# Optimization experiments

Hardware: AMD Instinct MI355X
Metric: run time of the kernel (lower is better)

The kernel has to match this reference:

```python
import jax, jax.numpy as jnp
import numpy as np

EMBED_DIM = 1024
HEAD_SIZE = 128
B, S = 8, 2048

def setup_inputs() -> dict:
    rng = jax.random.key(0)
    k1, k2, k3, k4, k5, k6 = jax.random.split(rng, 6)
    std = 1.0 / EMBED_DIM  # nn.initializers.normal(stddev=1/embed_dim)
    return {
        "key": jax.random.normal(k1, (B, S, EMBED_DIM), dtype=jnp.float32),
        "query": jax.random.normal(k2, (B, S, EMBED_DIM), dtype=jnp.float32),
        "value": jax.random.normal(k3, (B, S, EMBED_DIM), dtype=jnp.float32),
        "W_Q": jax.random.normal(k4, (EMBED_DIM, HEAD_SIZE), dtype=jnp.float32) * std,
        "W_K": jax.random.normal(k5, (EMBED_DIM, HEAD_SIZE), dtype=jnp.float32) * std,
        "W_V": jax.random.normal(k6, (EMBED_DIM, HEAD_SIZE), dtype=jnp.float32) * std,
    }

def reference(key, query, value, W_Q, W_K, W_V):
    # Parallel retention: (Q K^T * causal_mask) V
    q_proj = query @ W_Q        # (B, S, H)
    k_proj = key @ W_K          # (B, S, H)
    v_proj = value @ W_V        # (B, S, H)
    ret = jnp.einsum("bsh,bth->bst", q_proj, k_proj)  # (B, S, S)
    # full_self_retention=False -> lower-triangular (causal) mask
    decay_matrix = jnp.tril(jnp.ones((S, S), dtype=ret.dtype))
    ret = ret * decay_matrix
    return ret @ v_proj          # (B, S, H)
```

## Files before the change

### kernel.cpp

```cpp
#include <hip/hip_runtime.h>
#include <cstdint>

#define B_  8
#define S_  2048
#define E_  1024
#define H_  128
#define NC_ 16

typedef __attribute__((ext_vector_type(8))) short bf16x8;
typedef __attribute__((ext_vector_type(4))) float f32x4;

__device__ __forceinline__ short f2bf(float f){
  uint32_t u = __builtin_bit_cast(uint32_t, f);
  u = (u + 0x7fffu + ((u >> 16) & 1u)) >> 16;
  return (short)u;
}
__device__ __forceinline__ float bf2f(short s){
  uint32_t u = ((uint32_t)(uint16_t)s) << 16;
  return __builtin_bit_cast(float, u);
}

__global__ __launch_bounds__(256) void wt_kernel(
    const float* __restrict__ WQ, const float* __restrict__ WK,
    const float* __restrict__ WV,
    short* __restrict__ WtQ, short* __restrict__ WtK, short* __restrict__ WtV)
{
  int which = blockIdx.z;
  const float* W = which == 0 ? WQ : which == 1 ? WK : WV;
  short* Wt      = which == 0 ? WtQ : which == 1 ? WtK : WtV;
  int k0 = blockIdx.x * 32, n0 = blockIdx.y * 32;
  __shared__ float t[32][33];
  int tx = threadIdx.x & 31, ty = threadIdx.x >> 5;
  #pragma unroll
  for (int i = 0; i < 4; i++)
    t[ty + i * 8][tx] = W[(size_t)(k0 + ty + i * 8) * H_ + n0 + tx];
  __syncthreads();
  #pragma unroll
  for (int i = 0; i < 4; i++)
    Wt[(size_t)(n0 + ty + i * 8) * E_ + k0 + tx] = f2bf(t[tx][ty + i * 8]);
}

__global__ __launch_bounds__(256) void proj_kernel(
    const float* __restrict__ Xq, const float* __restrict__ Xk,
    const float* __restrict__ Xv,
    const short* __restrict__ Wtq, const short* __restrict__ Wtk,
    const short* __restrict__ Wtv,
    short* __restrict__ q, short* __restrict__ k,
    short* __restrict__ kT, short* __restrict__ vT)
{
  int which = blockIdx.y;
  const float* X  = which == 0 ? Xq  : which == 1 ? Xk  : Xv;
  const short* Wt = which == 0 ? Wtq : which == 1 ? Wtk : Wtv;

  int tid = threadIdx.x, lane = tid & 63, wave = tid >> 6;
  int lr = lane & 15, lq = lane >> 4;
  int rowbase = blockIdx.x * 64 + wave * 16;

  __shared__ short Bs[2][128 * 72];

  const float* xr = X + (size_t)(rowbase + lr) * E_ + lq * 8;

  f32x4 acc[8];
  #pragma unroll
  for (int tn = 0; tn < 8; tn++) acc[tn] = (f32x4){0.f, 0.f, 0.f, 0.f};

  bf16x8 bst[4];
  f32x4  a0[4], a1[4];

  #pragma unroll
  for (int v = 0; v < 4; v++){
    int c = v * 256 + tid;
    int n = c >> 3, off = (c & 7) * 8;
    bst[v] = *(const bf16x8*)(Wt + (size_t)n * E_ + off);
  }
  #pragma unroll
  for (int s = 0; s < 2; s++){
    a0[2 * s]     = *(const f32x4*)(xr + s * 32);
    a0[2 * s + 1] = *(const f32x4*)(xr + s * 32 + 4);
  }
  #pragma unroll
  for (int v = 0; v < 4; v++){
    int c = v * 256 + tid;
    int n = c >> 3, off = (c & 7) * 8;
    *(bf16x8*)(&Bs[0][n * 72 + off]) = bst[v];
  }
  __syncthreads();

  for (int t = 0; t < 16; t++){
    const int cur = t & 1;
    if (t < 15){
      #pragma unroll
      for (int v = 0; v < 4; v++){
        int c = v * 256 + tid;
        int n = c >> 3, off = (c & 7) * 8;
        bst[v] = *(const bf16x8*)(Wt + (size_t)n * E_ + (t + 1) * 64 + off);
      }
      #pragma unroll
      for (int s = 0; s < 2; s++){
        a1[2 * s]     = *(const f32x4*)(xr + (t + 1) * 64 + s * 32);
        a1[2 * s + 1] = *(const f32x4*)(xr + (t + 1) * 64 + s * 32 + 4);
      }
    }
    #pragma unroll
    for (int s = 0; s < 2; s++){
      bf16x8 a;
      #pragma unroll
      for (int j = 0; j < 4; j++){
        a[j] = f2bf(a0[2 * s][j]); a[4 + j] = f2bf(a0[2 * s + 1][j]);
      }
      #pragma unroll
      for (int tn = 0; tn < 8; tn++){
        bf16x8 bfr = *(const bf16x8*)(&Bs[cur][(tn * 16 + lr) * 72 + s * 32 + lq * 8]);
        acc[tn] = __builtin_amdgcn_mfma_f32_16x16x32_bf16(a, bfr, acc[tn], 0, 0, 0);
      }
    }
    if (t < 15){
      #pragma unroll
      for (int v = 0; v < 4; v++){
        int c = v * 256 + tid;
        int n = c >> 3, off = (c & 7) * 8;
        *(bf16x8*)(&Bs[cur ^ 1][n * 72 + off]) = bst[v];
      }
      #pragma unroll
      for (int i2 = 0; i2 < 4; i2++) a0[i2] = a1[i2];
      __syncthreads();
    }
  }

  if (which <= 1){
    short* P = which == 0 ? q : k;
    #pragma unroll
    for (int tn = 0; tn < 8; tn++)
      #pragma unroll
      for (int r4 = 0; r4 < 4; r4++)
        P[(size_t)(rowbase + lq * 4 + r4) * H_ + tn * 16 + lr] = f2bf(acc[tn][r4]);
  }
  if (which >= 1){
    short* T = which == 1 ? kT : vT;
    int b = rowbase >> 11, srow = rowbase & 2047;
    #pragma unroll
    for (int tn = 0; tn < 8; tn++){
      union { short sh[4]; uint2 u; } pk;
      #pragma unroll
      for (int r4 = 0; r4 < 4; r4++) pk.sh[r4] = f2bf(acc[tn][r4]);
      *(uint2*)(T + ((size_t)b * H_ + tn * 16 + lr) * S_ + srow + lq * 4) = pk.u;
    }
  }
}

__global__ __launch_bounds__(256) void chunk_state(
    const short* __restrict__ vT, const short* __restrict__ kT,
    float* __restrict__ M)
{
  int j = blockIdx.x, half = blockIdx.y, b = blockIdx.z;
  int tid = threadIdx.x, lane = tid & 63, wave = tid >> 6;
  int wrow = wave * 32;
  int lr = lane & 15, lq = lane >> 4;

  __shared__ short As[128 * 136];
  __shared__ short Bs[64 * 136];

  const short* vtb = vT + (size_t)b * H_ * S_ + j * 128;
  const short* ktb = kT + (size_t)b * H_ * S_ + (size_t)half * 64 * S_ + j * 128;

  #pragma unroll
  for (int v = 0; v < 8; v++){
    int c = v * 256 + tid;
    int r = c >> 4, off = (c & 15) * 8;
    *(bf16x8*)(&As[r * 136 + off]) = *(const bf16x8*)(vtb + (size_t)r * S_ + off);
  }
  #pragma unroll
  for (int v = 0; v < 4; v++){
    int c = v * 256 + tid;
    int r = c >> 4, off = (c & 15) * 8;
    *(bf16x8*)(&Bs[r * 136 + off]) = *(const bf16x8*)(ktb + (size_t)r * S_ + off);
  }
  __syncthreads();

  f32x4 acc[2][4];
  #pragma unroll
  for (int a = 0; a < 2; a++)
    #pragma unroll
    for (int c = 0; c < 4; c++) acc[a][c] = (f32x4){0.f, 0.f, 0.f, 0.f};

  #pragma unroll
  for (int s = 0; s < 4; s++){
    int t0 = s * 32;
    bf16x8 af[2], bf[4];
    #pragma unroll
    for (int tm = 0; tm < 2; tm++)
      af[tm] = *(const bf16x8*)(&As[(wrow + tm * 16 + lr) * 136 + t0 + lq * 8]);
    #pragma unroll
    for (int tn = 0; tn < 4; tn++)
      bf[tn] = *(const bf16x8*)(&Bs[(tn * 16 + lr) * 136 + t0 + lq * 8]);
    #pragma unroll
    for (int tm = 0; tm < 2; tm++)
      #pragma unroll
      for (int tn = 0; tn < 4; tn++)
        acc[tm][tn] = __builtin_amdgcn_mfma_f32_16x16x32_bf16(
            af[tm], bf[tn], acc[tm][tn], 0, 0, 0);
  }

  float* mb = M + (size_t)(b * NC_ + j) * 16384;
  #pragma unroll
  for (int tm = 0; tm < 2; tm++)
    #pragma unroll
    for (int tn = 0; tn < 4; tn++)
      #pragma unroll
      for (int r4 = 0; r4 < 4; r4++){
        int row = wrow + tm * 16 + lq * 4 + r4;
        int col = half * 64 + tn * 16 + lr;
        mb[row * 128 + col] = acc[tm][tn][r4];
      }
}

__global__ __launch_bounds__(256) void prefix_state(
    const float* __restrict__ M, short* __restrict__ Shi, short* __restrict__ Slo)
{
  int b = blockIdx.y;
  int idx = (blockIdx.x * 256 + threadIdx.x) * 2;
  float2 mv[NC_];
  #pragma unroll
  for (int j = 0; j < NC_; j++)
    mv[j] = *(const float2*)(M + (size_t)(b * NC_ + j) * 16384 + idx);

  float r0 = 0.f, r1 = 0.f;
  #pragma unroll
  for (int j = 0; j < NC_; j++){
    size_t o = (size_t)(b * NC_ + j) * 16384 + idx;
    short h0 = f2bf(r0), h1 = f2bf(r1);
    short l0 = f2bf(r0 - bf2f(h0)), l1 = f2bf(r1 - bf2f(h1));
    union { short s[2]; uint32_t u; } ph, pl;
    ph.s[0] = h0; ph.s[1] = h1;
    pl.s[0] = l0; pl.s[1] = l1;
    *(uint32_t*)(Shi + o) = ph.u;
    *(uint32_t*)(Slo + o) = pl.u;
    r0 += mv[j].x; r1 += mv[j].y;
  }
}

__global__ __launch_bounds__(256) void passC(
    const short* __restrict__ qb, const short* __restrict__ kb,
    const short* __restrict__ vT, const short* __restrict__ Shi,
    const short* __restrict__ Slo, float* __restrict__ out)
{
  int i = blockIdx.x, half = blockIdx.y, b = blockIdx.z;
  int roff = half * 64;
  int tid = threadIdx.x, lane = tid & 63, wave = tid >> 6;
  int wrow = (wave >> 1) * 32, wcol = (wave & 1) * 64;
  int lr = lane & 15, lq = lane >> 4;

  __shared__ short Ss[64 * 136];
  __shared__ short Bt0[128 * 136];
  __shared__ short Bt1[128 * 136];

  const short* qbase = qb + ((size_t)b * S_ + i * 128 + roff) * H_;
  const short* kbase = kb + ((size_t)b * S_ + i * 128) * H_;
  const short* vtb   = vT + (size_t)b * H_ * S_ + i * 128;
  const short* shib  = Shi + (size_t)(b * NC_ + i) * 16384;
  const short* slob  = Slo + (size_t)(b * NC_ + i) * 16384;

  bf16x8 kst[8], vst[8], hst[8], lst[8];
  #pragma unroll
  for (int v = 0; v < 8; v++){
    int c = v * 256 + tid;
    int r = c >> 4, off = (c & 15) * 8;
    kst[v] = *(const bf16x8*)(kbase + (size_t)r * H_ + off);
    vst[v] = *(const bf16x8*)(vtb  + (size_t)r * S_ + off);
    hst[v] = *(const bf16x8*)(shib + (size_t)r * 128 + off);
    lst[v] = *(const bf16x8*)(slob + (size_t)r * 128 + off);
  }
  bf16x8 aq[2][4];
  #pragma unroll
  for (int tm = 0; tm < 2; tm++)
    #pragma unroll
    for (int hs = 0; hs < 4; hs++)
      aq[tm][hs] = *(const bf16x8*)(
          qbase + (size_t)(wrow + tm * 16 + lr) * H_ + hs * 32 + lq * 8);

  #pragma unroll
  for (int v = 0; v < 8; v++){
    int c = v * 256 + tid;
    int r = c >> 4, off = (c & 15) * 8;
    *(bf16x8*)(&Bt0[r * 136 + off]) = kst[v];
  }
  __syncthreads();

  f32x4 acc[2][4];
  #pragma unroll
  for (int a = 0; a < 2; a++)
    #pragma unroll
    for (int c = 0; c < 4; c++) acc[a][c] = (f32x4){0.f, 0.f, 0.f, 0.f};

  #pragma unroll
  for (int hs = 0; hs < 4; hs++){
    bf16x8 bf[4];
    #pragma unroll
    for (int tn = 0; tn < 4; tn++)
      bf[tn] = *(const bf16x8*)(&Bt0[(wcol + tn * 16 + lr) * 136 + hs * 32 + lq * 8]);
    #pragma unroll
    for (int tm = 0; tm < 2; tm++)
      #pragma unroll
      for (int tn = 0; tn < 4; tn++)
        acc[tm][tn] = __builtin_amdgcn_mfma_f32_16x16x32_bf16(
            aq[tm][hs], bf[tn], acc[tm][tn], 0, 0, 0);
  }

  #pragma unroll
  for (int tm = 0; tm < 2; tm++)
    #pragma unroll
    for (int tn = 0; tn < 4; tn++)
      #pragma unroll
      for (int r4 = 0; r4 < 4; r4++){
        int row = wrow + tm * 16 + lq * 4 + r4;
        int col = wcol + tn * 16 + lr;
        float vv = (col <= roff + row) ? acc[tm][tn][r4] : 0.f;
        Ss[row * 136 + col] = f2bf(vv);
      }
  #pragma unroll
  for (int v = 0; v < 8; v++){
    int c = v * 256 + tid;
    int r = c >> 4, off = (c & 15) * 8;
    *(bf16x8*)(&Bt1[r * 136 + off]) = vst[v];
  }
  #pragma unroll
  for (int a = 0; a < 2; a++)
    #pragma unroll
    for (int c = 0; c < 4; c++) acc[a][c] = (f32x4){0.f, 0.f, 0.f, 0.f};
  __syncthreads();

  #pragma unroll
  for (int s = 0; s < 4; s++){
    int t0 = s * 32;
    bf16x8 af[2], bf[4];
    #pragma unroll
    for (int tm = 0; tm < 2; tm++)
      af[tm] = *(const bf16x8*)(&Ss[(wrow + tm * 16 + lr) * 136 + t0 + lq * 8]);
    #pragma unroll
    for (int tn = 0; tn < 4; tn++)
      bf[tn] = *(const bf16x8*)(&Bt1[(wcol + tn * 16 + lr) * 136 + t0 + lq * 8]);
    #pragma unroll
    for (int tm = 0; tm < 2; tm++)
      #pragma unroll
      for (int tn = 0; tn < 4; tn++)
        acc[tm][tn] = __builtin_amdgcn_mfma_f32_16x16x32_bf16(
            af[tm], bf[tn], acc[tm][tn], 0, 0, 0);
  }
  #pragma unroll
  for (int v = 0; v < 8; v++){
    int c = v * 256 + tid;
    int r = c >> 4, off = (c & 15) * 8;
    *(bf16x8*)(&Bt0[r * 136 + off]) = hst[v];
  }
  __syncthreads();

  #pragma unroll
  for (int hs = 0; hs < 4; hs++){
    bf16x8 bf[4];
    #pragma unroll
    for (int tn = 0; tn < 4; tn++)
      bf[tn] = *(const bf16x8*)(&Bt0[(wcol + tn * 16 + lr) * 136 + hs * 32 + lq * 8]);
    #pragma unroll
    for (int tm = 0; tm < 2; tm++)
      #pragma unroll
      for (int tn = 0; tn < 4; tn++)
        acc[tm][tn] = __builtin_amdgcn_mfma_f32_16x16x32_bf16(
            aq[tm][hs], bf[tn], acc[tm][tn], 0, 0, 0);
  }
  #pragma unroll
  for (int v = 0; v < 8; v++){
    int c = v * 256 + tid;
    int r = c >> 4, off = (c & 15) * 8;
    *(bf16x8*)(&Bt1[r * 136 + off]) = lst[v];
  }
  __syncthreads();

  #pragma unroll
  for (int hs = 0; hs < 4; hs++){
    bf16x8 bf[4];
    #pragma unroll
    for (int tn = 0; tn < 4; tn++)
      bf[tn] = *(const bf16x8*)(&Bt1[(wcol + tn * 16 + lr) * 136 + hs * 32 + lq * 8]);
    #pragma unroll
    for (int tm = 0; tm < 2; tm++)
      #pragma unroll
      for (int tn = 0; tn < 4; tn++)
        acc[tm][tn] = __builtin_amdgcn_mfma_f32_16x16x32_bf16(
            aq[tm][hs], bf[tn], acc[tm][tn], 0, 0, 0);
  }

  float* ob = out + ((size_t)b * S_ + i * 128 + roff) * H_;
  #pragma unroll
  for (int tm = 0; tm < 2; tm++)
    #pragma unroll
    for (int tn = 0; tn < 4; tn++)
      #pragma unroll
      for (int r4 = 0; r4 < 4; r4++){
        int row = wrow + tm * 16 + lq * 4 + r4;
        int col = wcol + tn * 16 + lr;
        ob[(size_t)row * H_ + col] = acc[tm][tn][r4];
      }
}

extern "C" void kernel_launch(void* const* d_in, const int* in_sizes, int n_in,
                              void* d_out, int out_size, void* d_ws, size_t ws_size,
                              hipStream_t stream) {
  const float* key   = (const float*)d_in[0];
  const float* query = (const float*)d_in[1];
  const float* value = (const float*)d_in[2];
  const float* WQ    = (const float*)d_in[3];
  const float* WK    = (const float*)d_in[4];
  const float* WV    = (const float*)d_in[5];
  float* out = (float*)d_out;

  char* w = (char*)d_ws;
  short* WtQ = (short*)(w + 0);
  short* WtK = (short*)(w + 262144);
  short* WtV = (short*)(w + 524288);
  size_t o = 786432;
  short* q  = (short*)(w + o); o += 4194304;
  short* k  = (short*)(w + o); o += 4194304;
  short* kT = (short*)(w + o); o += 4194304;
  short* vT = (short*)(w + o); o += 4194304;
  float* M  = (float*)(w + o); o += 8388608;
  short* Shi= (short*)(w + o); o += 4194304;
  short* Slo= (short*)(w + o); o += 4194304;

  wt_kernel   <<<dim3(32, 4, 3),       256, 0, stream>>>(WQ, WK, WV, WtQ, WtK, WtV);
  proj_kernel <<<dim3(256, 3),         256, 0, stream>>>(query, key, value,
                                                         WtQ, WtK, WtV, q, k, kT, vT);
  chunk_state <<<dim3(NC_, 2, B_),     256, 0, stream>>>(vT, kT, M);
  prefix_state<<<dim3(32, B_),         256, 0, stream>>>(M, Shi, Slo);
  passC       <<<dim3(NC_, 2, B_),     256, 0, stream>>>(q, k, vT, Shi, Slo, out);
}
```

Before: 239.2 us.

## Drop LDS staging in projection and split chunk kernels into quarter tiles

The projection kernel now reads bf16 weight fragments straight from global memory (L2-resident) instead of double-buffering them through shared memory, which removes the barriers and LDS traffic. It also loads 128-wide K chunks per iteration. chunk_state and passC now split each 128-row chunk into four 32-row pieces instead of two 64-row pieces, doubling the grid (256 to 512 blocks) so the 256 CUs are better occupied. In exchange, passC re-stages the full K, V and state tiles four times per chunk, and the projection kernel makes more scattered global reads.

```diff
diff --git a/kernel.cpp b/kernel.cpp
--- a/kernel.cpp
+++ b/kernel.cpp
@@ -56,74 +56,34 @@
   int lr = lane & 15, lq = lane >> 4;
   int rowbase = blockIdx.x * 64 + wave * 16;
 
-  __shared__ short Bs[2][128 * 72];
-
   const float* xr = X + (size_t)(rowbase + lr) * E_ + lq * 8;
+  const short* wb = Wt + (size_t)lr * E_ + lq * 8;
 
   f32x4 acc[8];
   #pragma unroll
   for (int tn = 0; tn < 8; tn++) acc[tn] = (f32x4){0.f, 0.f, 0.f, 0.f};
 
-  bf16x8 bst[4];
-  f32x4  a0[4], a1[4];
-
-  #pragma unroll
-  for (int v = 0; v < 4; v++){
-    int c = v * 256 + tid;
-    int n = c >> 3, off = (c & 7) * 8;
-    bst[v] = *(const bf16x8*)(Wt + (size_t)n * E_ + off);
-  }
-  #pragma unroll
-  for (int s = 0; s < 2; s++){
-    a0[2 * s]     = *(const f32x4*)(xr + s * 32);
-    a0[2 * s + 1] = *(const f32x4*)(xr + s * 32 + 4);
-  }
-  #pragma unroll
-  for (int v = 0; v < 4; v++){
-    int c = v * 256 + tid;
-    int n = c >> 3, off = (c & 7) * 8;
-    *(bf16x8*)(&Bs[0][n * 72 + off]) = bst[v];
-  }
-  __syncthreads();
-
-  for (int t = 0; t < 16; t++){
-    const int cur = t & 1;
-    if (t < 15){
-      #pragma unroll
-      for (int v = 0; v < 4; v++){
-        int c = v * 256 + tid;
-        int n = c >> 3, off = (c & 7) * 8;
-        bst[v] = *(const bf16x8*)(Wt + (size_t)n * E_ + (t + 1) * 64 + off);
-      }
-      #pragma unroll
-      for (int s = 0; s < 2; s++){
-        a1[2 * s]     = *(const f32x4*)(xr + (t + 1) * 64 + s * 32);
-        a1[2 * s + 1] = *(const f32x4*)(xr + (t + 1) * 64 + s * 32 + 4);
-      }
+  #pragma unroll 2
+  for (int kc = 0; kc < 8; kc++){
+    f32x4 ar[8];
+    #pragma unroll
+    for (int s = 0; s < 4; s++){
+      ar[2 * s]     = *(const f32x4*)(xr + kc * 128 + s * 32);
+      ar[2 * s + 1] = *(const f32x4*)(xr + kc * 128 + s * 32 + 4);
     }
     #pragma unroll
-    for (int s = 0; s < 2; s++){
+    for (int s = 0; s < 4; s++){
       bf16x8 a;
       #pragma unroll
       for (int j = 0; j < 4; j++){
-        a[j] = f2bf(a0[2 * s][j]); a[4 + j] = f2bf(a0[2 * s + 1][j]);
+        a[j] = f2bf(ar[2 * s][j]); a[4 + j] = f2bf(ar[2 * s + 1][j]);
       }
       #pragma unroll
       for (int tn = 0; tn < 8; tn++){
-        bf16x8 bfr = *(const bf16x8*)(&Bs[cur][(tn * 16 + lr) * 72 + s * 32 + lq * 8]);
+        bf16x8 bfr = *(const bf16x8*)(
+            wb + (size_t)(tn * 16) * E_ + kc * 128 + s * 32);
         acc[tn] = __builtin_amdgcn_mfma_f32_16x16x32_bf16(a, bfr, acc[tn], 0, 0, 0);
       }
-    }
-    if (t < 15){
-      #pragma unroll
-      for (int v = 0; v < 4; v++){
-        int c = v * 256 + tid;
-        int n = c >> 3, off = (c & 7) * 8;
-        *(bf16x8*)(&Bs[cur ^ 1][n * 72 + off]) = bst[v];
-      }
-      #pragma unroll
-      for (int i2 = 0; i2 < 4; i2++) a0[i2] = a1[i2];
-      __syncthreads();
     }
   }
 
@@ -152,16 +112,16 @@
     const short* __restrict__ vT, const short* __restrict__ kT,
     float* __restrict__ M)
 {
-  int j = blockIdx.x, half = blockIdx.y, b = blockIdx.z;
+  int j = blockIdx.x, qtr = blockIdx.y, b = blockIdx.z;
   int tid = threadIdx.x, lane = tid & 63, wave = tid >> 6;
   int wrow = wave * 32;
   int lr = lane & 15, lq = lane >> 4;
 
   __shared__ short As[128 * 136];
-  __shared__ short Bs[64 * 136];
+  __shared__ short Bs[32 * 136];
 
   const short* vtb = vT + (size_t)b * H_ * S_ + j * 128;
-  const short* ktb = kT + (size_t)b * H_ * S_ + (size_t)half * 64 * S_ + j * 128;
+  const short* ktb = kT + (size_t)b * H_ * S_ + (size_t)qtr * 32 * S_ + j * 128;
 
   #pragma unroll
   for (int v = 0; v < 8; v++){
@@ -170,33 +130,33 @@
     *(bf16x8*)(&As[r * 136 + off]) = *(const bf16x8*)(vtb + (size_t)r * S_ + off);
   }
   #pragma unroll
-  for (int v = 0; v < 4; v++){
+  for (int v = 0; v < 2; v++){
     int c = v * 256 + tid;
     int r = c >> 4, off = (c & 15) * 8;
     *(bf16x8*)(&Bs[r * 136 + off]) = *(const bf16x8*)(ktb + (size_t)r * S_ + off);
   }
   __syncthreads();
 
-  f32x4 acc[2][4];
+  f32x4 acc[2][2];
   #pragma unroll
   for (int a = 0; a < 2; a++)
     #pragma unroll
-    for (int c = 0; c < 4; c++) acc[a][c] = (f32x4){0.f, 0.f, 0.f, 0.f};
+    for (int c = 0; c < 2; c++) acc[a][c] = (f32x4){0.f, 0.f, 0.f, 0.f};
 
   #pragma unroll
   for (int s = 0; s < 4; s++){
     int t0 = s * 32;
-    bf16x8 af[2], bf[4];
+    bf16x8 af[2], bf[2];
     #pragma unroll
     for (int tm = 0; tm < 2; tm++)
       af[tm] = *(const bf16x8*)(&As[(wrow + tm * 16 + lr) * 136 + t0 + lq * 8]);
     #pragma unroll
-    for (int tn = 0; tn < 4; tn++)
+    for (int tn = 0; tn < 2; tn++)
       bf[tn] = *(const bf16x8*)(&Bs[(tn * 16 + lr) * 136 + t0 + lq * 8]);
     #pragma unroll
     for (int tm = 0; tm < 2; tm++)
       #pragma unroll
-      for (int tn = 0; tn < 4; tn++)
+      for (int tn = 0; tn < 2; tn++)
         acc[tm][tn] = __builtin_amdgcn_mfma_f32_16x16x32_bf16(
             af[tm], bf[tn], acc[tm][tn], 0, 0, 0);
   }
@@ -205,11 +165,11 @@
   #pragma unroll
   for (int tm = 0; tm < 2; tm++)
     #pragma unroll
-    for (int tn = 0; tn < 4; tn++)
+    for (int tn = 0; tn < 2; tn++)
       #pragma unroll
       for (int r4 = 0; r4 < 4; r4++){
         int row = wrow + tm * 16 + lq * 4 + r4;
-        int col = half * 64 + tn * 16 + lr;
+        int col = qtr * 32 + tn * 16 + lr;
         mb[row * 128 + col] = acc[tm][tn][r4];
       }
 }
@@ -244,13 +204,13 @@
     const short* __restrict__ vT, const short* __restrict__ Shi,
     const short* __restrict__ Slo, float* __restrict__ out)
 {
-  int i = blockIdx.x, half = blockIdx.y, b = blockIdx.z;
-  int roff = half * 64;
+  int i = blockIdx.x, qtr = blockIdx.y, b = blockIdx.z;
+  int roff = qtr * 32;
   int tid = threadIdx.x, lane = tid & 63, wave = tid >> 6;
-  int wrow = (wave >> 1) * 32, wcol = (wave & 1) * 64;
+  int wcol = wave * 32;
   int lr = lane & 15, lq = lane >> 4;
 
-  __shared__ short Ss[64 * 136];
+  __shared__ short Ss[32 * 136];
   __shared__ short Bt0[128 * 136];
   __shared__ short Bt1[128 * 136];
 
@@ -276,7 +236,7 @@
     #pragma unroll
     for (int hs = 0; hs < 4; hs++)
       aq[tm][hs] = *(const bf16x8*)(
-          qbase + (size_t)(wrow + tm * 16 + lr) * H_ + hs * 32 + lq * 8);
+          qbase + (size_t)(tm * 16 + lr) * H_ + hs * 32 + lq * 8);
 
   #pragma unroll
   for (int v = 0; v < 8; v++){
@@ -286,117 +246,118 @@
   }
   __syncthreads();
 
-  f32x4 acc[2][4];
+  f32x4 accS[2][2];
   #pragma unroll
   for (int a = 0; a < 2; a++)
     #pragma unroll
-    for (int c = 0; c < 4; c++) acc[a][c] = (f32x4){0.f, 0.f, 0.f, 0.f};
+    for (int c = 0; c < 2; c++) accS[a][c] = (f32x4){0.f, 0.f, 0.f, 0.f};
 
   #pragma unroll
   for (int hs = 0; hs < 4; hs++){
-    bf16x8 bf[4];
-    #pragma unroll
-    for (int tn = 0; tn < 4; tn++)
+    bf16x8 bf[2];
+    #pragma unroll
+    for (int tn = 0; tn < 2; tn++)
       bf[tn] = *(const bf16x8*)(&Bt0[(wcol + tn * 16 + lr) * 136 + hs * 32 + lq * 8]);
     #pragma unroll
     for (int tm = 0; tm < 2; tm++)
       #pragma unroll
-      for (int tn = 0; tn < 4; tn++)
+      for (int tn = 0; tn < 2; tn++)
+        accS[tm][tn] = __builtin_amdgcn_mfma_f32_16x16x32_bf16(
+            aq[tm][hs], bf[tn], accS[tm][tn], 0, 0, 0);
+  }
+
+  #pragma unroll
+  for (int tm = 0; tm < 2; tm++)
+    #pragma unroll
+    for (int tn = 0; tn < 2; tn++)
+      #pragma unroll
+      for (int r4 = 0; r4 < 4; r4++){
+        int row = tm * 16 + lq * 4 + r4;
+        int col = wcol + tn * 16 + lr;
+        float vv = (col <= roff + row) ? accS[tm][tn][r4] : 0.f;
+        Ss[row * 136 + col] = f2bf(vv);
+      }
+  #pragma unroll
+  for (int v = 0; v < 8; v++){
+    int c = v * 256 + tid;
+    int r = c >> 4, off = (c & 15) * 8;
+    *(bf16x8*)(&Bt1[r * 136 + off]) = vst[v];
+  }
+  f32x4 acc[2][2];
+  #pragma unroll
+  for (int a = 0; a < 2; a++)
+    #pragma unroll
+    for (int c = 0; c < 2; c++) acc[a][c] = (f32x4){0.f, 0.f, 0.f, 0.f};
+  __syncthreads();
+
+  #pragma unroll
+  for (int s = 0; s < 4; s++){
+    int t0 = s * 32;
+    bf16x8 af[2], bf[2];
+    #pragma unroll
+    for (int tm = 0; tm < 2; tm++)
+      af[tm] = *(const bf16x8*)(&Ss[(tm * 16 + lr) * 136 + t0 + lq * 8]);
+    #pragma unroll
+    for (int tn = 0; tn < 2; tn++)
+      bf[tn] = *(const bf16x8*)(&Bt1[(wcol + tn * 16 + lr) * 136 + t0 + lq * 8]);
+    #pragma unroll
+    for (int tm = 0; tm < 2; tm++)
+      #pragma unroll
+      for (int tn = 0; tn < 2; tn++)
+        acc[tm][tn] = __builtin_amdgcn_mfma_f32_16x16x32_bf16(
+            af[tm], bf[tn], acc[tm][tn], 0, 0, 0);
+  }
+  #pragma unroll
+  for (int v = 0; v < 8; v++){
+    int c = v * 256 + tid;
+    int r = c >> 4, off = (c & 15) * 8;
+    *(bf16x8*)(&Bt0[r * 136 + off]) = hst[v];
+  }
+  __syncthreads();
+
+  #pragma unroll
+  for (int hs = 0; hs < 4; hs++){
+    bf16x8 bf[2];
+    #pragma unroll
+    for (int tn = 0; tn < 2; tn++)
+      bf[tn] = *(const bf16x8*)(&Bt0[(wcol + tn * 16 + lr) * 136 + hs * 32 + lq * 8]);
+    #pragma unroll
+    for (int tm = 0; tm < 2; tm++)
+      #pragma unroll
+      for (int tn = 0; tn < 2; tn++)
         acc[tm][tn] = __builtin_amdgcn_mfma_f32_16x16x32_bf16(
             aq[tm][hs], bf[tn], acc[tm][tn], 0, 0, 0);
   }
-
-  #pragma unroll
-  for (int tm = 0; tm < 2; tm++)
-    #pragma unroll
-    for (int tn = 0; tn < 4; tn++)
-      #pragma unroll
-      for (int r4 = 0; r4 < 4; r4++){
-        int row = wrow + tm * 16 + lq * 4 + r4;
-        int col = wcol + tn * 16 + lr;
-        float vv = (col <= roff + row) ? acc[tm][tn][r4] : 0.f;
-        Ss[row * 136 + col] = f2bf(vv);
-      }
-  #pragma unroll
-  for (int v = 0; v < 8; v++){
-    int c = v * 256 + tid;
-    int r = c >> 4, off = (c & 15) * 8;
-    *(bf16x8*)(&Bt1[r * 136 + off]) = vst[v];
-  }
-  #pragma unroll
-  for (int a = 0; a < 2; a++)
-    #pragma unroll
-    for (int c = 0; c < 4; c++) acc[a][c] = (f32x4){0.f, 0.f, 0.f, 0.f};
-  __syncthreads();
-
-  #pragma unroll
-  for (int s = 0; s < 4; s++){
-    int t0 = s * 32;
-    bf16x8 af[2], bf[4];
-    #pragma unroll
-    for (int tm = 0; tm < 2; tm++)
-      af[tm] = *(const bf16x8*)(&Ss[(wrow + tm * 16 + lr) * 136 + t0 + lq * 8]);
-    #pragma unroll
-    for (int tn = 0; tn < 4; tn++)
-      bf[tn] = *(const bf16x8*)(&Bt1[(wcol + tn * 16 + lr) * 136 + t0 + lq * 8]);
-    #pragma unroll
-    for (int tm = 0; tm < 2; tm++)
-      #pragma unroll
-      for (int tn = 0; tn < 4; tn++)
-        acc[tm][tn] = __builtin_amdgcn_mfma_f32_16x16x32_bf16(
-            af[tm], bf[tn], acc[tm][tn], 0, 0, 0);
-  }
-  #pragma unroll
-  for (int v = 0; v < 8; v++){
-    int c = v * 256 + tid;
-    int r = c >> 4, off = (c & 15) * 8;
-    *(bf16x8*)(&Bt0[r * 136 + off]) = hst[v];
+  #pragma unroll
+  for (int v = 0; v < 8; v++){
+    int c = v * 256 + tid;
+    int r = c >> 4, off = (c & 15) * 8;
+    *(bf16x8*)(&Bt1[r * 136 + off]) = lst[v];
   }
   __syncthreads();
 
   #pragma unroll
   for (int hs = 0; hs < 4; hs++){
-    bf16x8 bf[4];
-    #pragma unroll
-    for (int tn = 0; tn < 4; tn++)
-      bf[tn] = *(const bf16x8*)(&Bt0[(wcol + tn * 16 + lr) * 136 + hs * 32 + lq * 8]);
-    #pragma unroll
-    for (int tm = 0; tm < 2; tm++)
-      #pragma unroll
-      for (int tn = 0; tn < 4; tn++)
+    bf16x8 bf[2];
+    #pragma unroll
+    for (int tn = 0; tn < 2; tn++)
+      bf[tn] = *(const bf16x8*)(&Bt1[(wcol + tn * 16 + lr) * 136 + hs * 32 + lq * 8]);
+    #pragma unroll
+    for (int tm = 0; tm < 2; tm++)
+      #pragma unroll
+      for (int tn = 0; tn < 2; tn++)
         acc[tm][tn] = __builtin_amdgcn_mfma_f32_16x16x32_bf16(
             aq[tm][hs], bf[tn], acc[tm][tn], 0, 0, 0);
   }
-  #pragma unroll
-  for (int v = 0; v < 8; v++){
-    int c = v * 256 + tid;
-    int r = c >> 4, off = (c & 15) * 8;
-    *(bf16x8*)(&Bt1[r * 136 + off]) = lst[v];
-  }
-  __syncthreads();
-
-  #pragma unroll
-  for (int hs = 0; hs < 4; hs++){
-    bf16x8 bf[4];
-    #pragma unroll
-    for (int tn = 0; tn < 4; tn++)
-      bf[tn] = *(const bf16x8*)(&Bt1[(wcol + tn * 16 + lr) * 136 + hs * 32 + lq * 8]);
-    #pragma unroll
-    for (int tm = 0; tm < 2; tm++)
-      #pragma unroll
-      for (int tn = 0; tn < 4; tn++)
-        acc[tm][tn] = __builtin_amdgcn_mfma_f32_16x16x32_bf16(
-            aq[tm][hs], bf[tn], acc[tm][tn], 0, 0, 0);
-  }
 
   float* ob = out + ((size_t)b * S_ + i * 128 + roff) * H_;
   #pragma unroll
   for (int tm = 0; tm < 2; tm++)
     #pragma unroll
-    for (int tn = 0; tn < 4; tn++)
+    for (int tn = 0; tn < 2; tn++)
       #pragma unroll
       for (int r4 = 0; r4 < 4; r4++){
-        int row = wrow + tm * 16 + lq * 4 + r4;
+        int row = tm * 16 + lq * 4 + r4;
         int col = wcol + tn * 16 + lr;
         ob[(size_t)row * H_ + col] = acc[tm][tn][r4];
       }
@@ -429,7 +390,7 @@
   wt_kernel   <<<dim3(32, 4, 3),       256, 0, stream>>>(WQ, WK, WV, WtQ, WtK, WtV);
   proj_kernel <<<dim3(256, 3),         256, 0, stream>>>(query, key, value,
                                                          WtQ, WtK, WtV, q, k, kT, vT);
-  chunk_state <<<dim3(NC_, 2, B_),     256, 0, stream>>>(vT, kT, M);
+  chunk_state <<<dim3(NC_, 4, B_),     256, 0, stream>>>(vT, kT, M);
   prefix_state<<<dim3(32, B_),         256, 0, stream>>>(M, Shi, Slo);
-  passC       <<<dim3(NC_, 2, B_),     256, 0, stream>>>(q, k, vT, Shi, Slo, out);
-}
+  passC       <<<dim3(NC_, 4, B_),     256, 0, stream>>>(q, k, vT, Shi, Slo, out);
+}
```

New measurement: 288.7 us. 1.21x slower.
